# Kernel optimization log

Hardware: AMD Instinct MI355X
Metric: run time of the kernel (lower is better)

The kernel has to match this reference:

```python
import jax, jax.numpy as jnp
import numpy as np

B, C, H, W = 4, 512, 64, 64
NUM_GROUPS = 32
EPS = 1e-6


def setup_inputs() -> dict:
    key = jax.random.key(0)
    ks = jax.random.split(key, 5)
    s = 1.0 / np.sqrt(C)
    return {
        "x": jax.random.normal(ks[0], (B, C, H, W), dtype=jnp.float32),
        "gn_scale": jnp.ones((C,), jnp.float32),
        "gn_bias": jnp.zeros((C,), jnp.float32),
        "wq": jax.random.normal(ks[1], (C, C), jnp.float32) * s,
        "bq": jnp.zeros((C,), jnp.float32),
        "wk": jax.random.normal(ks[2], (C, C), jnp.float32) * s,
        "bk": jnp.zeros((C,), jnp.float32),
        "wv": jax.random.normal(ks[3], (C, C), jnp.float32) * s,
        "bv": jnp.zeros((C,), jnp.float32),
        "wo": jax.random.normal(ks[4], (C, C), jnp.float32) * s,
        "bo": jnp.zeros((C,), jnp.float32),
    }


def _group_norm(x, scale, bias):
    # x: [b, c, h, w]; normalize over (c//g, h, w) within each of g groups
    b, c, h, w = x.shape
    g = NUM_GROUPS
    xg = x.reshape(b, g, c // g, h, w)
    mean = jnp.mean(xg, axis=(2, 3, 4), keepdims=True)
    var = jnp.var(xg, axis=(2, 3, 4), keepdims=True)
    xg = (xg - mean) * jax.lax.rsqrt(var + EPS)
    xn = xg.reshape(b, c, h, w)
    return xn * scale[None, :, None, None] + bias[None, :, None, None]


def _conv1x1(x, w, b):
    # channel-mixing 1x1 conv: [b, c, h, w] x [c_in, c_out] -> [b, c_out, h, w]
    return jnp.einsum('bchw,cd->bdhw', x, w) + b[None, :, None, None]


def reference(x, gn_scale, gn_bias, wq, bq, wk, bk, wv, bv, wo, bo):
    b, c, h, w = x.shape
    h_ = _group_norm(x, gn_scale, gn_bias)
    q = _conv1x1(h_, wq, bq).reshape(b, c, h * w).transpose(0, 2, 1)  # [b, hw, c]
    k = _conv1x1(h_, wk, bk).reshape(b, c, h * w)                     # [b, c, hw]
    v = _conv1x1(h_, wv, bv).reshape(b, c, h * w)                     # [b, c, hw]
    scores = jnp.matmul(q, k) * (c ** -0.5)      # [b, hw, hw]
    attn = jax.nn.softmax(scores, axis=-1)       # [b, hw, hw]
    out = jnp.matmul(v, attn.transpose(0, 2, 1)) # [b, c, hw]
    out = out.reshape(b, c, h, w)
    out = _conv1x1(out, wo, bo)
    return x + out
```

## Files before the change

kernel.cpp:

```cpp
#include <hip/hip_runtime.h>
#include <stdint.h>

typedef __attribute__((ext_vector_type(8))) short short8;
typedef __attribute__((ext_vector_type(4))) float f32x4;
typedef __attribute__((ext_vector_type(16))) float f32x16;
typedef __attribute__((ext_vector_type(2))) unsigned int uint2v;

__device__ __forceinline__ short cvt_bf16(float f) {
  uint32_t u = __builtin_bit_cast(uint32_t, f);
  u += 0x7FFFu + ((u >> 16) & 1u);
  return (short)(u >> 16);
}

__device__ __forceinline__ float bf16_to_f32(short s) {
  return __builtin_bit_cast(float, (uint32_t)((unsigned short)s) << 16);
}

__device__ __forceinline__ void gload_lds16(const void* g, void* l) {
  __builtin_amdgcn_global_load_lds(
      (const __attribute__((address_space(1))) void*)g,
      (__attribute__((address_space(3))) void*)l, 16, 0, 0);
}

__global__ __launch_bounds__(256) void k_transpose_w(const float* __restrict__ src,
                                                     short* __restrict__ dst) {
  __shared__ float t[32][33];
  int n0 = blockIdx.x * 32, c0 = blockIdx.y * 32;
  int lx = threadIdx.x & 31, ly = threadIdx.x >> 5;
#pragma unroll
  for (int i = 0; i < 4; ++i) {
    int c = ly + i * 8;
    t[c][lx] = src[(size_t)(c0 + c) * 512 + n0 + lx];
  }
  __syncthreads();
#pragma unroll
  for (int i = 0; i < 4; ++i) {
    int n = ly + i * 8;
    dst[(size_t)(n0 + n) * 512 + c0 + lx] = cvt_bf16(t[lx][n]);
  }
}

__global__ void k_bias_concat(const float* __restrict__ bq, const float* __restrict__ bk,
                              float* __restrict__ bqk) {
  int i = blockIdx.x * 256 + threadIdx.x;
  if (i < 512) bqk[i] = bq[i];
  else if (i < 1024) bqk[i] = bk[i - 512];
}

__global__ __launch_bounds__(256) void k_gn_stats(const float* __restrict__ x,
                                                  float* __restrict__ stats) {
  int bg = blockIdx.x;
  const float* p = x + (size_t)bg * 65536;
  float s = 0.f, ss = 0.f;
#pragma unroll 4
  for (int i = 0; i < 64; ++i) {
    float4 v = *(const float4*)(p + i * 1024 + threadIdx.x * 4);
    s += v.x + v.y + v.z + v.w;
    ss += v.x * v.x + v.y * v.y + v.z * v.z + v.w * v.w;
  }
#pragma unroll
  for (int m = 1; m < 64; m <<= 1) {
    s += __shfl_xor(s, m, 64);
    ss += __shfl_xor(ss, m, 64);
  }
  __shared__ float red[8];
  int w = threadIdx.x >> 6;
  if ((threadIdx.x & 63) == 0) { red[w * 2] = s; red[w * 2 + 1] = ss; }
  __syncthreads();
  if (threadIdx.x == 0) {
    float S1 = red[0] + red[2] + red[4] + red[6];
    float S2 = red[1] + red[3] + red[5] + red[7];
    float mean = S1 * (1.f / 65536.f);
    float var = S2 * (1.f / 65536.f) - mean * mean;
    stats[bg * 2] = mean;
    stats[bg * 2 + 1] = rsqrtf(var + 1e-6f);
  }
}

__global__ __launch_bounds__(256) void k_gn_apply(const float* __restrict__ x,
    const float* __restrict__ stats, const float* __restrict__ gsc,
    const float* __restrict__ gbi, short* __restrict__ h_t) {
  __shared__ float t[64][65];
  int p0 = blockIdx.x * 64, c0 = blockIdx.y * 64, b = blockIdx.z;
  int lp = threadIdx.x & 63, lc = threadIdx.x >> 6;
#pragma unroll
  for (int i = 0; i < 16; ++i) {
    int c = c0 + lc * 16 + i;
    float mean = stats[(b * 32 + (c >> 4)) * 2];
    float rstd = stats[(b * 32 + (c >> 4)) * 2 + 1];
    float v = x[((size_t)b * 512 + c) * 4096 + p0 + lp];
    t[lc * 16 + i][lp] = (v - mean) * rstd * gsc[c] + gbi[c];
  }
  __syncthreads();
  int pl = threadIdx.x >> 2;
  int cs = (threadIdx.x & 3) * 16;
  short8 v8a, v8b;
#pragma unroll
  for (int j = 0; j < 8; ++j) v8a[j] = cvt_bf16(t[cs + j][pl]);
#pragma unroll
  for (int j = 0; j < 8; ++j) v8b[j] = cvt_bf16(t[cs + 8 + j][pl]);
  size_t o = ((size_t)(b * 4096 + p0 + pl)) * 512 + c0 + cs;
  *(short8*)(h_t + o) = v8a;
  *(short8*)(h_t + o + 8) = v8b;
}

template <int BIAS_M, int FINAL>
__global__ __launch_bounds__(256) void k_gemm(const short* __restrict__ A,
    const short* __restrict__ Bm, const float* __restrict__ bias,
    short* __restrict__ Cb, float* __restrict__ Cf, const float* __restrict__ resid,
    int ldc) {
  __shared__ __align__(16) short a_lds[128 * 32];
  __shared__ __align__(16) short b_lds[128 * 32];
  int m0 = blockIdx.x * 128, n0 = blockIdx.y * 128;
  int lane = threadIdx.x & 63, wid = threadIdx.x >> 6;
  int h16 = lane >> 4, l16 = lane & 15;
  int wr = wid >> 1, wc = wid & 1;
  int srow = lane >> 2, sslot = lane & 3;

  f32x4 acc[4][4];
#pragma unroll
  for (int mi = 0; mi < 4; ++mi)
#pragma unroll
    for (int ni = 0; ni < 4; ++ni) acc[mi][ni] = (f32x4){0.f, 0.f, 0.f, 0.f};

  for (int kk = 0; kk < 16; ++kk) {
#pragma unroll
    for (int i = 0; i < 2; ++i) {
      int r0 = (wid * 2 + i) * 16;
      gload_lds16(A + ((size_t)(m0 + r0 + srow)) * 512 + kk * 32 + sslot * 8, a_lds + r0 * 32);
      gload_lds16(Bm + ((size_t)(n0 + r0 + srow)) * 512 + kk * 32 + sslot * 8, b_lds + r0 * 32);
    }
    asm volatile("s_waitcnt vmcnt(0)" ::: "memory");
    __syncthreads();
    short8 af[4], bf[4];
#pragma unroll
    for (int mi = 0; mi < 4; ++mi)
      af[mi] = *(const short8*)(a_lds + (wr * 64 + mi * 16 + l16) * 32 + h16 * 8);
#pragma unroll
    for (int ni = 0; ni < 4; ++ni)
      bf[ni] = *(const short8*)(b_lds + (wc * 64 + ni * 16 + l16) * 32 + h16 * 8);
#pragma unroll
    for (int mi = 0; mi < 4; ++mi)
#pragma unroll
      for (int ni = 0; ni < 4; ++ni)
        acc[mi][ni] = __builtin_amdgcn_mfma_f32_16x16x32_bf16(af[mi], bf[ni], acc[mi][ni], 0, 0, 0);
    __syncthreads();
  }

#pragma unroll
  for (int mi = 0; mi < 4; ++mi)
#pragma unroll
    for (int ni = 0; ni < 4; ++ni)
#pragma unroll
      for (int r = 0; r < 4; ++r) {
        int row = m0 + wr * 64 + mi * 16 + 4 * h16 + r;
        int col = n0 + wc * 64 + ni * 16 + l16;
        float v = acc[mi][ni][r] + (BIAS_M ? bias[row] : bias[col]);
        if (FINAL) {
          size_t oidx = ((size_t)((col >> 12) * 512 + row)) * 4096 + (col & 4095);
          Cf[oidx] = v + resid[oidx];
        } else {
          Cb[(size_t)row * ldc + col] = cvt_bf16(v);
        }
      }
}

__global__ __launch_bounds__(512, 2) void k_flash2(const short* __restrict__ qk,
    const short* __restrict__ v_t, short* __restrict__ oa, short* __restrict__ ob,
    float* __restrict__ ml) {
  __shared__ __align__(16) short k_lds[32 * 512];
  __shared__ __align__(16) short v_lds[512 * 64];
  __shared__ __align__(16) float s_lds[8 * 1024];
  __shared__ __align__(16) short p_lds[128 * 40];

  const int tid = threadIdx.x;
  const int lane = tid & 63, wid = tid >> 6;
  const int qg = wid >> 1, dh = wid & 1;
  const int l31 = lane & 31, h = lane >> 5;
  const int bx = blockIdx.x;
  const int combo = bx & 7, qt = bx >> 3;
  const int b = combo >> 1, s = combo & 1;
  const float K2 = 0.06376649f;

  short8 qf[16];
  {
    const short* qbase = qk + ((size_t)(b * 4096 + qt * 128 + qg * 32 + l31)) * 1024
                         + dh * 256 + h * 8;
#pragma unroll
    for (int ks = 0; ks < 16; ++ks) qf[ks] = *(const short8*)(qbase + ks * 16);
  }
  asm volatile("s_waitcnt vmcnt(0)" ::: "memory");

  const size_t kvrow0 = (size_t)(b * 4096 + s * 2048);

#define STAGE_K(T)                                                                    \
  {                                                                                   \
    int t_ = (T);                                                                     \
    _Pragma("unroll") for (int i = 0; i < 4; ++i) {                                   \
      int row = wid * 4 + i;                                                          \
      gload_lds16(qk + (kvrow0 + t_ * 32 + row) * 1024 + 512 + ((lane ^ (row & 7)) * 8), \
                  k_lds + row * 512);                                                 \
    }                                                                                 \
  }
#define STAGE_V(P)                                                                    \
  {                                                                                   \
    int p_ = (P);                                                                     \
    _Pragma("unroll") for (int ii = 0; ii < 8; ++ii) {                                \
      int d = wid * 64 + ii * 8 + (lane >> 3);                                        \
      gload_lds16(v_t + (size_t)d * 16384 + (b * 4096 + s * 2048 + p_ * 64)           \
                      + (((lane & 7) ^ (d & 7)) * 8),                                 \
                  v_lds + (wid * 8 + ii) * 512);                                      \
    }                                                                                 \
  }

  STAGE_K(0);
  STAGE_V(0);
  asm volatile("s_waitcnt vmcnt(8)" ::: "memory");
  __builtin_amdgcn_s_barrier();
  __builtin_amdgcn_sched_barrier(0);

  float m_run = -3.0e38f, l_run = 0.f;
  f32x16 acc[8];
#pragma unroll
  for (int tl = 0; tl < 8; ++tl)
#pragma unroll
    for (int r = 0; r < 16; ++r) acc[tl][r] = 0.f;

  for (int t = 0; t < 64; ++t) {
    f32x16 st;
#pragma unroll
    for (int r = 0; r < 16; ++r) st[r] = 0.f;
#pragma unroll
    for (int ks = 0; ks < 16; ++ks) {
      int c = dh * 32 + ks * 2 + h;
      short8 kf = *(const short8*)(k_lds + l31 * 512 + ((c ^ (l31 & 7)) * 8));
      st = __builtin_amdgcn_mfma_f32_32x32x16_bf16(kf, qf[ks], st, 0, 0, 0);
    }
    {
      float* sp = s_lds + wid * 1024 + lane * 4;
#pragma unroll
      for (int q4 = 0; q4 < 4; ++q4) {
        f32x4 v = {st[q4 * 4 + 0], st[q4 * 4 + 1], st[q4 * 4 + 2], st[q4 * 4 + 3]};
        *(f32x4*)(sp + q4 * 256) = v;
      }
    }
    asm volatile("s_waitcnt lgkmcnt(0)" ::: "memory");
    __builtin_amdgcn_s_barrier();
    __builtin_amdgcn_sched_barrier(0);
    STAGE_K(t + 1 < 64 ? t + 1 : 63);
    {
      const float* sp = s_lds + (wid ^ 1) * 1024 + lane * 4;
#pragma unroll
      for (int q4 = 0; q4 < 4; ++q4) {
        f32x4 v = *(const f32x4*)(sp + q4 * 256);
        st[q4 * 4 + 0] += v[0]; st[q4 * 4 + 1] += v[1];
        st[q4 * 4 + 2] += v[2]; st[q4 * 4 + 3] += v[3];
      }
    }
    float mt = st[0];
#pragma unroll
    for (int r = 1; r < 16; ++r) mt = fmaxf(mt, st[r]);
    mt = fmaxf(mt, __shfl_xor(mt, 32));
    if (__any(mt > m_run + 45.0f)) {
      float mnew = fmaxf(m_run, mt);
      float rs = exp2f((m_run - mnew) * K2);
      m_run = mnew;
      l_run *= rs;
#pragma unroll
      for (int r = 0; r < 16; ++r) {
        int rowq = (r & 3) + 8 * (r >> 2) + 4 * h;
        float rr = __shfl(rs, rowq);
#pragma unroll
        for (int tl = 0; tl < 8; ++tl) acc[tl][r] *= rr;
      }
    }
    float ls = 0.f;
#pragma unroll
    for (int r = 0; r < 16; ++r) { st[r] = exp2f((st[r] - m_run) * K2); ls += st[r]; }
    ls += __shfl_xor(ls, 32);
    l_run += ls;
    if (dh == 0) {
      int q = qg * 32 + l31;
#pragma unroll
      for (int g = 0; g < 4; ++g) {
        unsigned int p0, p1;
        asm("v_cvt_pk_bf16_f32 %0, %1, %2" : "=v"(p0) : "v"(st[4 * g + 0]), "v"(st[4 * g + 1]));
        asm("v_cvt_pk_bf16_f32 %0, %1, %2" : "=v"(p1) : "v"(st[4 * g + 2]), "v"(st[4 * g + 3]));
        uint2v w; w[0] = p0; w[1] = p1;
        *(uint2v*)(p_lds + q * 40 + g * 8 + h * 4) = w;
      }
    }
    asm volatile("s_waitcnt vmcnt(4) lgkmcnt(0)" ::: "memory");
    __builtin_amdgcn_s_barrier();
    __builtin_amdgcn_sched_barrier(0);
#pragma unroll
    for (int ks = 0; ks < 2; ++ks) {
      short8 pa = *(const short8*)(p_lds + (qg * 32 + l31) * 40 + ks * 16 + h * 8);
#pragma unroll
      for (int tl = 0; tl < 8; ++tl) {
        int d = dh * 256 + tl * 32 + l31;
        int c = (t & 1) * 4 + ks * 2 + h;
        short8 vb = *(const short8*)(v_lds + d * 64 + ((c ^ (d & 7)) * 8));
        acc[tl] = __builtin_amdgcn_mfma_f32_32x32x16_bf16(pa, vb, acc[tl], 0, 0, 0);
      }
    }
    asm volatile("s_waitcnt vmcnt(0) lgkmcnt(0)" ::: "memory");
    __builtin_amdgcn_s_barrier();
    __builtin_amdgcn_sched_barrier(0);
    if (t & 1) STAGE_V(((t + 1) >> 1) < 32 ? ((t + 1) >> 1) : 31);
  }

  float linv = 1.0f / l_run;
  short* obuf = (s == 0) ? oa : ob;
#pragma unroll
  for (int r = 0; r < 16; ++r) {
    int rowq = (r & 3) + 8 * (r >> 2) + 4 * h;
    float li = __shfl(linv, rowq);
    size_t grow = ((size_t)(b * 4096 + qt * 128 + qg * 32 + rowq)) * 512;
#pragma unroll
    for (int tl = 0; tl < 8; ++tl)
      obuf[grow + dh * 256 + tl * 32 + l31] = cvt_bf16(acc[tl][r] * li);
  }
  if (dh == 0 && lane < 32) {
    int gq = b * 4096 + qt * 128 + qg * 32 + lane;
    ml[((size_t)s * 16384 + gq) * 2 + 0] = m_run;
    ml[((size_t)s * 16384 + gq) * 2 + 1] = l_run;
  }
#undef STAGE_K
#undef STAGE_V
}

__global__ __launch_bounds__(256) void k_combine(const short* __restrict__ oa,
    const float* __restrict__ ml, short* __restrict__ ob_out) {
  int gq = blockIdx.x * 4 + (threadIdx.x >> 6);
  int d0 = (threadIdx.x & 63) * 8;
  const float K2 = 0.06376649f;
  float ma = ml[(size_t)gq * 2 + 0], la = ml[(size_t)gq * 2 + 1];
  float mb = ml[((size_t)16384 + gq) * 2 + 0], lb = ml[((size_t)16384 + gq) * 2 + 1];
  float m = fmaxf(ma, mb);
  float ca = exp2f((ma - m) * K2) * la;
  float cb = exp2f((mb - m) * K2) * lb;
  float inv = 1.f / (ca + cb);
  ca *= inv; cb *= inv;
  short8 a = *(const short8*)(oa + (size_t)gq * 512 + d0);
  short8 bv = *(const short8*)(ob_out + (size_t)gq * 512 + d0);
  short8 o;
#pragma unroll
  for (int j = 0; j < 8; ++j)
    o[j] = cvt_bf16(ca * bf16_to_f32(a[j]) + cb * bf16_to_f32(bv[j]));
  *(short8*)(ob_out + (size_t)gq * 512 + d0) = o;
}

extern "C" void kernel_launch(void* const* d_in, const int* in_sizes, int n_in,
                              void* d_out, int out_size, void* d_ws, size_t ws_size,
                              hipStream_t stream) {
  const float* x   = (const float*)d_in[0];
  const float* gsc = (const float*)d_in[1];
  const float* gbi = (const float*)d_in[2];
  const float* wq  = (const float*)d_in[3];
  const float* bq  = (const float*)d_in[4];
  const float* wk  = (const float*)d_in[5];
  const float* bk  = (const float*)d_in[6];
  const float* wv  = (const float*)d_in[7];
  const float* bv  = (const float*)d_in[8];
  const float* wo  = (const float*)d_in[9];
  const float* bo  = (const float*)d_in[10];
  float* out = (float*)d_out;

  char* ws = (char*)d_ws;
  float* stats = (float*)ws;
  float* bqk   = (float*)(ws + 4096);
  short* wqk_t = (short*)(ws + 16384);
  short* wv_t  = (short*)(ws + 16384 + (1u << 20));
  short* wo_t  = (short*)(ws + 16384 + (1u << 20) + (1u << 19));
  char*  big   = ws + 16384 + (1u << 21);
  short* h_t   = (short*)big;
  short* qkb   = (short*)(big + (16ll << 20));
  short* v_t   = (short*)(big + (48ll << 20));
  short* o_at  = (short*)(big + (64ll << 20));
  float* mlbuf = (float*)(big + (80ll << 20));

  dim3 b256(256);
  k_transpose_w<<<dim3(16, 16), b256, 0, stream>>>(wq, wqk_t);
  k_transpose_w<<<dim3(16, 16), b256, 0, stream>>>(wk, wqk_t + 512 * 512);
  k_transpose_w<<<dim3(16, 16), b256, 0, stream>>>(wv, wv_t);
  k_transpose_w<<<dim3(16, 16), b256, 0, stream>>>(wo, wo_t);
  k_bias_concat<<<4, 256, 0, stream>>>(bq, bk, bqk);
  k_gn_stats<<<128, b256, 0, stream>>>(x, stats);
  k_gn_apply<<<dim3(64, 8, 4), b256, 0, stream>>>(x, stats, gsc, gbi, h_t);
  k_gemm<0, 0><<<dim3(128, 8), b256, 0, stream>>>(h_t, wqk_t, bqk, qkb, nullptr, nullptr, 1024);
  k_gemm<1, 0><<<dim3(4, 128), b256, 0, stream>>>(wv_t, h_t, bv, v_t, nullptr, nullptr, 16384);
  k_flash2<<<dim3(256), dim3(512), 0, stream>>>(qkb, v_t, h_t, o_at, mlbuf);
  k_combine<<<dim3(4096), b256, 0, stream>>>(h_t, mlbuf, o_at);
  k_gemm<1, 1><<<dim3(4, 128), b256, 0, stream>>>(wo_t, o_at, bo, nullptr, out, x, 0);
}
```

Baseline: 369.5 us.

## Store LDS tiles in MFMA fragment order and keep P in registers

```diff
diff --git a/kernel.cpp b/kernel.cpp
--- a/kernel.cpp
+++ b/kernel.cpp
@@ -4,7 +4,7 @@
 typedef __attribute__((ext_vector_type(8))) short short8;
 typedef __attribute__((ext_vector_type(4))) float f32x4;
 typedef __attribute__((ext_vector_type(16))) float f32x16;
-typedef __attribute__((ext_vector_type(2))) unsigned int uint2v;
+typedef __attribute__((ext_vector_type(4))) unsigned int uint4v;
 
 __device__ __forceinline__ short cvt_bf16(float f) {
   uint32_t u = __builtin_bit_cast(uint32_t, f);
@@ -115,7 +115,6 @@
   int lane = threadIdx.x & 63, wid = threadIdx.x >> 6;
   int h16 = lane >> 4, l16 = lane & 15;
   int wr = wid >> 1, wc = wid & 1;
-  int srow = lane >> 2, sslot = lane & 3;
 
   f32x4 acc[4][4];
 #pragma unroll
@@ -125,20 +124,23 @@
 
   for (int kk = 0; kk < 16; ++kk) {
 #pragma unroll
-    for (int i = 0; i < 2; ++i) {
-      int r0 = (wid * 2 + i) * 16;
-      gload_lds16(A + ((size_t)(m0 + r0 + srow)) * 512 + kk * 32 + sslot * 8, a_lds + r0 * 32);
-      gload_lds16(Bm + ((size_t)(n0 + r0 + srow)) * 512 + kk * 32 + sslot * 8, b_lds + r0 * 32);
+    for (int i = 0; i < 4; ++i) {
+      int idx = wid * 4 + i;
+      int mat = idx >> 3, h = (idx >> 1) & 3, rh = idx & 1;
+      const short* src = (mat ? Bm : A) +
+          ((size_t)((mat ? n0 : m0) + rh * 64 + lane)) * 512 + kk * 32 + h * 8;
+      short* dst = (mat ? b_lds : a_lds) + (h * 128 + rh * 64) * 8;
+      gload_lds16(src, dst);
     }
     asm volatile("s_waitcnt vmcnt(0)" ::: "memory");
     __syncthreads();
     short8 af[4], bf[4];
 #pragma unroll
     for (int mi = 0; mi < 4; ++mi)
-      af[mi] = *(const short8*)(a_lds + (wr * 64 + mi * 16 + l16) * 32 + h16 * 8);
+      af[mi] = *(const short8*)(a_lds + (h16 * 128 + wr * 64 + mi * 16 + l16) * 8);
 #pragma unroll
     for (int ni = 0; ni < 4; ++ni)
-      bf[ni] = *(const short8*)(b_lds + (wc * 64 + ni * 16 + l16) * 32 + h16 * 8);
+      bf[ni] = *(const short8*)(b_lds + (h16 * 128 + wc * 64 + ni * 16 + l16) * 8);
 #pragma unroll
     for (int mi = 0; mi < 4; ++mi)
 #pragma unroll
@@ -165,13 +167,12 @@
       }
 }
 
-__global__ __launch_bounds__(512, 2) void k_flash2(const short* __restrict__ qk,
+__global__ __launch_bounds__(512, 2) void k_flash3(const short* __restrict__ qk,
     const short* __restrict__ v_t, short* __restrict__ oa, short* __restrict__ ob,
     float* __restrict__ ml) {
   __shared__ __align__(16) short k_lds[32 * 512];
-  __shared__ __align__(16) short v_lds[512 * 64];
+  __shared__ __align__(16) short v_lds[32 * 512];
   __shared__ __align__(16) float s_lds[8 * 1024];
-  __shared__ __align__(16) short p_lds[128 * 40];
 
   const int tid = threadIdx.x;
   const int lane = tid & 63, wid = tid >> 6;
@@ -187,35 +188,35 @@
     const short* qbase = qk + ((size_t)(b * 4096 + qt * 128 + qg * 32 + l31)) * 1024
                          + dh * 256 + h * 8;
 #pragma unroll
-    for (int ks = 0; ks < 16; ++ks) qf[ks] = *(const short8*)(qbase + ks * 16);
-  }
-  asm volatile("s_waitcnt vmcnt(0)" ::: "memory");
+    for (int s_ = 0; s_ < 16; ++s_) qf[s_] = *(const short8*)(qbase + s_ * 16);
+  }
 
   const size_t kvrow0 = (size_t)(b * 4096 + s * 2048);
 
-#define STAGE_K(T)                                                                    \
+#define STAGE_K3(T)                                                                   \
   {                                                                                   \
     int t_ = (T);                                                                     \
     _Pragma("unroll") for (int i = 0; i < 4; ++i) {                                   \
-      int row = wid * 4 + i;                                                          \
-      gload_lds16(qk + (kvrow0 + t_ * 32 + row) * 1024 + 512 + ((lane ^ (row & 7)) * 8), \
-                  k_lds + row * 512);                                                 \
+      int ks = wid * 4 + i;                                                           \
+      gload_lds16(qk + (kvrow0 + t_ * 32 + l31) * 1024 + 512 + ks * 16 + h * 8,       \
+                  k_lds + ks * 512);                                                  \
     }                                                                                 \
   }
-#define STAGE_V(P)                                                                    \
+#define STAGE_V3(T)                                                                   \
   {                                                                                   \
-    int p_ = (P);                                                                     \
-    _Pragma("unroll") for (int ii = 0; ii < 8; ++ii) {                                \
-      int d = wid * 64 + ii * 8 + (lane >> 3);                                        \
-      gload_lds16(v_t + (size_t)d * 16384 + (b * 4096 + s * 2048 + p_ * 64)           \
-                      + (((lane & 7) ^ (d & 7)) * 8),                                 \
-                  v_lds + (wid * 8 + ii) * 512);                                      \
+    int t_ = (T);                                                                     \
+    _Pragma("unroll") for (int i = 0; i < 4; ++i) {                                   \
+      int si = wid * 4 + i;                                                           \
+      int ks = si >> 4, d0 = si & 15;                                                 \
+      gload_lds16(v_t + (size_t)(d0 * 32 + l31) * 16384                               \
+                      + (kvrow0 + t_ * 32 + ks * 16 + h * 8),                         \
+                  v_lds + si * 512);                                                  \
     }                                                                                 \
   }
 
-  STAGE_K(0);
-  STAGE_V(0);
-  asm volatile("s_waitcnt vmcnt(8)" ::: "memory");
+  STAGE_K3(0);
+  STAGE_V3(0);
+  asm volatile("s_waitcnt vmcnt(0)" ::: "memory");
   __builtin_amdgcn_s_barrier();
   __builtin_amdgcn_sched_barrier(0);
 
@@ -227,14 +228,14 @@
     for (int r = 0; r < 16; ++r) acc[tl][r] = 0.f;
 
   for (int t = 0; t < 64; ++t) {
+    int tn = (t + 1 < 64) ? t + 1 : 63;
     f32x16 st;
 #pragma unroll
     for (int r = 0; r < 16; ++r) st[r] = 0.f;
 #pragma unroll
-    for (int ks = 0; ks < 16; ++ks) {
-      int c = dh * 32 + ks * 2 + h;
-      short8 kf = *(const short8*)(k_lds + l31 * 512 + ((c ^ (l31 & 7)) * 8));
-      st = __builtin_amdgcn_mfma_f32_32x32x16_bf16(kf, qf[ks], st, 0, 0, 0);
+    for (int s_ = 0; s_ < 16; ++s_) {
+      short8 kf = *(const short8*)(k_lds + ((dh * 16 + s_) * 64 + lane) * 8);
+      st = __builtin_amdgcn_mfma_f32_32x32x16_bf16(kf, qf[s_], st, 0, 0, 0);
     }
     {
       float* sp = s_lds + wid * 1024 + lane * 4;
@@ -244,10 +245,10 @@
         *(f32x4*)(sp + q4 * 256) = v;
       }
     }
-    asm volatile("s_waitcnt lgkmcnt(0)" ::: "memory");
+    asm volatile("s_waitcnt vmcnt(0) lgkmcnt(0)" ::: "memory");
     __builtin_amdgcn_s_barrier();
     __builtin_amdgcn_sched_barrier(0);
-    STAGE_K(t + 1 < 64 ? t + 1 : 63);
+    STAGE_K3(tn);
     {
       const float* sp = s_lds + (wid ^ 1) * 1024 + lane * 4;
 #pragma unroll
@@ -279,35 +280,31 @@
     for (int r = 0; r < 16; ++r) { st[r] = exp2f((st[r] - m_run) * K2); ls += st[r]; }
     ls += __shfl_xor(ls, 32);
     l_run += ls;
-    if (dh == 0) {
-      int q = qg * 32 + l31;
-#pragma unroll
-      for (int g = 0; g < 4; ++g) {
-        unsigned int p0, p1;
-        asm("v_cvt_pk_bf16_f32 %0, %1, %2" : "=v"(p0) : "v"(st[4 * g + 0]), "v"(st[4 * g + 1]));
-        asm("v_cvt_pk_bf16_f32 %0, %1, %2" : "=v"(p1) : "v"(st[4 * g + 2]), "v"(st[4 * g + 3]));
-        uint2v w; w[0] = p0; w[1] = p1;
-        *(uint2v*)(p_lds + q * 40 + g * 8 + h * 4) = w;
-      }
-    }
-    asm volatile("s_waitcnt vmcnt(4) lgkmcnt(0)" ::: "memory");
-    __builtin_amdgcn_s_barrier();
-    __builtin_amdgcn_sched_barrier(0);
+    short8 pa[2];
 #pragma unroll
     for (int ks = 0; ks < 2; ++ks) {
-      short8 pa = *(const short8*)(p_lds + (qg * 32 + l31) * 40 + ks * 16 + h * 8);
+      unsigned int a0, a1, a2, a3;
+      int bse = ks * 8;
+      asm("v_cvt_pk_bf16_f32 %0, %1, %2" : "=v"(a0) : "v"(st[bse + 0]), "v"(st[bse + 1]));
+      asm("v_cvt_pk_bf16_f32 %0, %1, %2" : "=v"(a1) : "v"(st[bse + 2]), "v"(st[bse + 3]));
+      asm("v_cvt_pk_bf16_f32 %0, %1, %2" : "=v"(a2) : "v"(st[bse + 4]), "v"(st[bse + 5]));
+      asm("v_cvt_pk_bf16_f32 %0, %1, %2" : "=v"(a3) : "v"(st[bse + 6]), "v"(st[bse + 7]));
+      asm("v_permlane32_swap_b32 %0, %1" : "+v"(a0), "+v"(a2));
+      asm("v_permlane32_swap_b32 %0, %1" : "+v"(a1), "+v"(a3));
+      uint4v w; w[0] = a0; w[1] = a1; w[2] = a2; w[3] = a3;
+      pa[ks] = __builtin_bit_cast(short8, w);
+    }
+#pragma unroll
+    for (int ks = 0; ks < 2; ++ks)
 #pragma unroll
       for (int tl = 0; tl < 8; ++tl) {
-        int d = dh * 256 + tl * 32 + l31;
-        int c = (t & 1) * 4 + ks * 2 + h;
-        short8 vb = *(const short8*)(v_lds + d * 64 + ((c ^ (d & 7)) * 8));
-        acc[tl] = __builtin_amdgcn_mfma_f32_32x32x16_bf16(pa, vb, acc[tl], 0, 0, 0);
-      }
-    }
+        short8 vb = *(const short8*)(v_lds + ((ks * 16 + dh * 8 + tl) * 64 + lane) * 8);
+        acc[tl] = __builtin_amdgcn_mfma_f32_32x32x16_bf16(pa[ks], vb, acc[tl], 0, 0, 0);
+      }
     asm volatile("s_waitcnt vmcnt(0) lgkmcnt(0)" ::: "memory");
     __builtin_amdgcn_s_barrier();
     __builtin_amdgcn_sched_barrier(0);
-    if (t & 1) STAGE_V(((t + 1) >> 1) < 32 ? ((t + 1) >> 1) : 31);
+    STAGE_V3(tn);
   }
 
   float linv = 1.0f / l_run;
@@ -326,8 +323,8 @@
     ml[((size_t)s * 16384 + gq) * 2 + 0] = m_run;
     ml[((size_t)s * 16384 + gq) * 2 + 1] = l_run;
   }
-#undef STAGE_K
-#undef STAGE_V
+#undef STAGE_K3
+#undef STAGE_V3
 }
 
 __global__ __launch_bounds__(256) void k_combine(const short* __restrict__ oa,
@@ -390,7 +387,7 @@
   k_gn_apply<<<dim3(64, 8, 4), b256, 0, stream>>>(x, stats, gsc, gbi, h_t);
   k_gemm<0, 0><<<dim3(128, 8), b256, 0, stream>>>(h_t, wqk_t, bqk, qkb, nullptr, nullptr, 1024);
   k_gemm<1, 0><<<dim3(4, 128), b256, 0, stream>>>(wv_t, h_t, bv, v_t, nullptr, nullptr, 16384);
-  k_flash2<<<dim3(256), dim3(512), 0, stream>>>(qkb, v_t, h_t, o_at, mlbuf);
+  k_flash3<<<dim3(256), dim3(512), 0, stream>>>(qkb, v_t, h_t, o_at, mlbuf);
   k_combine<<<dim3(4096), b256, 0, stream>>>(h_t, mlbuf, o_at);
   k_gemm<1, 1><<<dim3(4, 128), b256, 0, stream>>>(wo_t, o_at, bo, nullptr, out, x, 0);
 }
```

New measurement: 382.7 us. 3.6% more time.
